# Optimization experiments

Measured on AMD Instinct MI355X. Metric: run time of the kernel, lower is better.

The kernel has to match this reference:

```python
import jax, jax.numpy as jnp
import numpy as np

EPS = 1e-12  # torch F.normalize clamp_min eps


def _agnn_conv(x, src, dst, beta, n):
    # x: [N, D]; src/dst: [E] (message flows src -> dst, softmax over dst's in-edges)
    xn = x / jnp.maximum(jnp.linalg.norm(x, axis=-1, keepdims=True), EPS)
    alpha = beta[0] * jnp.sum(xn[src] * xn[dst], axis=-1)            # [E] cosine sim * beta
    amax = jax.ops.segment_max(alpha, dst, num_segments=n)           # stable segment softmax
    ex = jnp.exp(alpha - amax[dst])
    denom = jax.ops.segment_sum(ex, dst, num_segments=n)
    w = ex / denom[dst]                                              # [E]
    return jax.ops.segment_sum(x[src] * w[:, None], dst, num_segments=n)


def setup_inputs() -> dict:
    key = jax.random.key(0)
    ks = jax.random.split(key, 8)
    N, E, G = 131072, 4194304, 2048
    x = jax.random.normal(ks[0], (N, 75), dtype=jnp.float32)
    edge_index = jax.random.randint(ks[1], (2, E), 0, N, dtype=jnp.int64)
    batch = jnp.sort(jax.random.randint(ks[2], (N,), 0, G, dtype=jnp.int64))
    lin1_w = jax.random.normal(ks[3], (16, 75), dtype=jnp.float32) * (1.0 / np.sqrt(75))
    lin1_b = jnp.zeros((16,), jnp.float32)
    beta1 = jnp.ones((1,), jnp.float32)   # prop1: requires_grad=False, beta=1
    beta2 = jnp.ones((1,), jnp.float32)   # prop2: learnable beta, init 1
    lin2_w = jax.random.normal(ks[4], (64, 16), dtype=jnp.float32) * (1.0 / np.sqrt(16))
    lin2_b = jnp.zeros((64,), jnp.float32)
    gather_w = jax.random.normal(ks[5], (1, 64), dtype=jnp.float32) * (1.0 / np.sqrt(64))
    gather_b = jnp.zeros((1,), jnp.float32)
    return {"x": x, "edge_index": edge_index, "batch": batch, "num_graphs": G,
            "lin1_w": lin1_w, "lin1_b": lin1_b, "beta1": beta1, "beta2": beta2,
            "lin2_w": lin2_w, "lin2_b": lin2_b, "gather_w": gather_w, "gather_b": gather_b}


def reference(x, edge_index, batch, num_graphs, lin1_w, lin1_b, beta1, beta2,
              lin2_w, lin2_b, gather_w, gather_b):
    n = x.shape[0]
    # PyG AGNNConv adds self-loops by default
    loops = jnp.arange(n, dtype=edge_index.dtype)
    src = jnp.concatenate([edge_index[0], loops])
    dst = jnp.concatenate([edge_index[1], loops])
    # dropout is identity in eval mode
    h = jax.nn.relu(x @ lin1_w.T + lin1_b)          # [N, 16]
    h = _agnn_conv(h, src, dst, beta1, n)
    h = _agnn_conv(h, src, dst, beta2, n)
    h = h @ lin2_w.T + lin2_b                        # [N, 64]
    y = jax.ops.segment_sum(h, batch, num_segments=num_graphs)  # global_add_pool [G, 64]
    return y @ gather_w.T + gather_b                 # [G, 1]
```

## Files before the change

kernel.cpp:

```cpp
#include <hip/hip_runtime.h>
#include <hip/hip_bf16.h>
#include <hip/hip_fp16.h>
#include <math.h>

#define SSEPS 1e-24f
#define NPB 256
#define NPB_SHIFT 8
#define SRC_BITS 17
#define SRC_MASK ((1 << SRC_BITS) - 1)
#define NB 512
#define CAP_B 8832
#define SC_EDGES 8192
#define SCB 512
#define SC_T 512
#define CSR_T 512

union QRowU { int2 v; _Float16 h[4]; };



__global__ void init_gcursor(int* g) {
    int i = threadIdx.x;
    if (i < NB) g[i] = i * CAP_B;
}

__global__ void init_out(float* out, const float* gb, int G) {
    int g = blockIdx.x * blockDim.x + threadIdx.x;
    if (g < G) out[g] = gb[0];
}

__global__ void compute_v(const float* l2w, const float* l2b, const float* gw,
                          float* vbuf) {
    int t = threadIdx.x;
    if (t < 16) {
        float a = 0.f;
        for (int j = 0; j < 64; ++j) a = fmaf(gw[j], l2w[j * 16 + t], a);
        vbuf[t] = a;
    } else if (t == 16) {
        float a = 0.f;
        for (int j = 0; j < 64; ++j) a = fmaf(gw[j], l2b[j], a);
        vbuf[16] = a;
    }
}

__global__ void lin1_relu(const float* __restrict__ x,
                          const float* __restrict__ W1,
                          const float* __restrict__ b1,
                          int* __restrict__ rec1, int N, int D) {
    __shared__ float Ws[16 * 75];
    __shared__ float Bs[16];
    for (int i = threadIdx.x; i < 16 * D; i += blockDim.x) Ws[i] = W1[i];
    if (threadIdx.x < 16) Bs[threadIdx.x] = b1[threadIdx.x];
    __syncthreads();

    int node = blockIdx.x * (blockDim.x >> 4) + (threadIdx.x >> 4);
    int c = threadIdx.x & 15;
    if (node >= N) return;

    const float* xr = x + (size_t)node * D;
    float acc = Bs[c];
    for (int k = 0; k < D; ++k) acc = fmaf(xr[k], Ws[c * D + k], acc);
    float h = fmaxf(acc, 0.f);

    float hn = __shfl_xor(h, 1);
    if (!(c & 1)) {
        union { _Float16 hh[2]; int i; } u;
        u.hh[0] = (_Float16)h;
        u.hh[1] = (_Float16)hn;
        rec1[8 * node + (c >> 1)] = u.i;
    }
}


__global__ __launch_bounds__(SC_T) void bucket_scatter(
    const int* __restrict__ src, const int* __restrict__ dst,
    int E, int* __restrict__ gcursor, int* __restrict__ packed) {
    __shared__ int lout[SC_EDGES];
    __shared__ int h[SCB];
    __shared__ int s[SCB];
    __shared__ int delta[SCB];
    int t = threadIdx.x;
    int base = blockIdx.x * SC_EDGES;
    int cnt = E - base;
    if (cnt > SC_EDGES) cnt = SC_EDGES;

    if (t < SCB) h[t] = 0;
    __syncthreads();
    for (int i = t; i < cnt; i += SC_T)
        atomicAdd(&h[dst[base + i] >> NPB_SHIFT], 1);
    __syncthreads();
    if (t < SCB) s[t] = h[t];
    __syncthreads();
    for (int off = 1; off < SCB; off <<= 1) {
        int a = (t < SCB && t >= off) ? s[t - off] : 0;
        __syncthreads();
        if (t < SCB) s[t] += a;
        __syncthreads();
    }
    if (t < SCB) {
        int c = h[t];
        int ex = s[t] - c;
        int gp = c ? atomicAdd(&gcursor[t], c) : 0;
        delta[t] = gp - ex;
        h[t] = ex;
    }
    __syncthreads();
    for (int i = t; i < cnt; i += SC_T) {
        int d = dst[base + i];
        int b = d >> NPB_SHIFT;
        int pos = atomicAdd(&h[b], 1);
        lout[pos] = ((d & (NPB - 1)) << SRC_BITS) | src[base + i];
    }
    __syncthreads();
    for (int i = t; i < cnt; i += SC_T) {
        int lo = 0, hi = SCB - 1;
        while (lo < hi) {
            int mid = (lo + hi) >> 1;
            if (s[mid] > i) hi = mid;
            else lo = mid + 1;
        }
        packed[delta[lo] + i] = lout[i];
    }
}

__global__ __launch_bounds__(CSR_T) void csr_build(
    const int* __restrict__ packed, const int* __restrict__ gcursor,
    int* __restrict__ deg, int* __restrict__ offs,
    int* __restrict__ csr_src, int N) {
    __shared__ int lout[CAP_B];
    __shared__ int ldeg[NPB];
    __shared__ int lofs[NPB];
    int b = blockIdx.x;
    int t = threadIdx.x;
    int e0 = b * CAP_B;
    int cnt = gcursor[b] - e0;
    if (t < NPB) ldeg[t] = 0;
    __syncthreads();
    for (int i = t; i < cnt; i += CSR_T)
        atomicAdd(&ldeg[packed[e0 + i] >> SRC_BITS], 1);
    __syncthreads();
    int v = (t < NPB) ? ldeg[t] : 0;
    if (t < NPB) lofs[t] = v;
    __syncthreads();
    for (int off = 1; off < NPB; off <<= 1) {
        int u = (t < NPB && t >= off) ? lofs[t - off] : 0;
        __syncthreads();
        if (t < NPB) lofs[t] += u;
        __syncthreads();
    }
    if (t < NPB) {
        int ex = lofs[t] - v;
        int node = (b << NPB_SHIFT) + t;
        if (node < N) {
            deg[node] = v;
            offs[node] = e0 + ex;
        }
        lofs[t] = ex;
    }
    __syncthreads();
    for (int i = t; i < cnt; i += CSR_T) {
        int p = packed[e0 + i];
        int pos = atomicAdd(&lofs[p >> SRC_BITS], 1);
        lout[pos] = p & SRC_MASK;
    }
    __syncthreads();
    for (int i = t; i < cnt; i += CSR_T)
        csr_src[e0 + i] = lout[i];
}

__global__ __launch_bounds__(256) void agnn_conv1(
    const int* __restrict__ rec1,
    const int* __restrict__ offs, const int* __restrict__ deg,
    const int* __restrict__ csr, const float* __restrict__ beta_p,
    int* __restrict__ rec2, int N) {
    int tid = blockIdx.x * blockDim.x + threadIdx.x;
    int node = tid >> 2;
    int q = tid & 3;
    if (node >= N) return;
    float beta = beta_p[0];
    const int2* rp = (const int2*)rec1;

    QRowU rdu;
    rdu.v = rp[4 * node + q];
    float xd[4];
#pragma unroll
    for (int k = 0; k < 4; ++k) xd[k] = (float)rdu.h[k];

    float ssd = 0.f;
#pragma unroll
    for (int k = 0; k < 4; ++k) ssd = fmaf(xd[k], xd[k], ssd);
    ssd += __shfl_xor(ssd, 1);
    ssd += __shfl_xor(ssd, 2);
    float invsd = rsqrtf(fmaxf(ssd, SSEPS));

    float e0 = __expf(beta * ssd * invsd * invsd);
    float denom = e0;
    float acc[4];
#pragma unroll
    for (int k = 0; k < 4; ++k) acc[k] = e0 * xd[k];

    int start = offs[node], cnt = deg[node];
    int i = 0;
    for (; i + 4 <= cnt; i += 4) {
        int j[4];
        QRowU r[4];
#pragma unroll
        for (int u = 0; u < 4; ++u) j[u] = __builtin_nontemporal_load(&csr[start + i + u]);
#pragma unroll
        for (int u = 0; u < 4; ++u) r[u].v = rp[4 * j[u] + q];
#pragma unroll
        for (int u = 0; u < 4; ++u) {
            float d = 0.f, ss = 0.f;
            float hs[4];
#pragma unroll
            for (int k = 0; k < 4; ++k) {
                hs[k] = (float)r[u].h[k];
                d = fmaf(xd[k], hs[k], d);
                ss = fmaf(hs[k], hs[k], ss);
            }
            d += __shfl_xor(d, 1);
            d += __shfl_xor(d, 2);
            ss += __shfl_xor(ss, 1);
            ss += __shfl_xor(ss, 2);
            float ee = __expf(beta * d * invsd * rsqrtf(fmaxf(ss, SSEPS)));
            denom += ee;
#pragma unroll
            for (int k = 0; k < 4; ++k) acc[k] = fmaf(ee, hs[k], acc[k]);
        }
    }
    for (; i < cnt; ++i) {
        int j = __builtin_nontemporal_load(&csr[start + i]);
        QRowU r;
        r.v = rp[4 * j + q];
        float d = 0.f, ss = 0.f;
        float hs[4];
#pragma unroll
        for (int k = 0; k < 4; ++k) {
            hs[k] = (float)r.h[k];
            d = fmaf(xd[k], hs[k], d);
            ss = fmaf(hs[k], hs[k], ss);
        }
        d += __shfl_xor(d, 1);
        d += __shfl_xor(d, 2);
        ss += __shfl_xor(ss, 1);
        ss += __shfl_xor(ss, 2);
        float ee = __expf(beta * d * invsd * rsqrtf(fmaxf(ss, SSEPS)));
        denom += ee;
#pragma unroll
        for (int k = 0; k < 4; ++k) acc[k] = fmaf(ee, hs[k], acc[k]);
    }

    float inv = 1.f / denom;
    QRowU w;
#pragma unroll
    for (int k = 0; k < 4; ++k) w.h[k] = (_Float16)(acc[k] * inv);
    ((int2*)rec2)[4 * node + q] = w.v;
}

__global__ __launch_bounds__(256) void agnn_conv2(
    const int* __restrict__ rec2,
    const int* __restrict__ offs, const int* __restrict__ deg,
    const int* __restrict__ csr, const float* __restrict__ beta_p,
    const float* __restrict__ vbuf,
    float* __restrict__ rbuf, int N) {
    int tid = blockIdx.x * blockDim.x + threadIdx.x;
    int node = tid >> 2;
    int q = tid & 3;
    if (node >= N) return;
    float beta = beta_p[0];
    const int2* rp = (const int2*)rec2;

    float vq[4];
#pragma unroll
    for (int k = 0; k < 4; ++k) vq[k] = vbuf[4 * q + k];

    QRowU rdu;
    rdu.v = rp[4 * node + q];
    float xd[4];
#pragma unroll
    for (int k = 0; k < 4; ++k) xd[k] = (float)rdu.h[k];

    float ssd = 0.f, pd = 0.f;
#pragma unroll
    for (int k = 0; k < 4; ++k) {
        ssd = fmaf(xd[k], xd[k], ssd);
        pd = fmaf(vq[k], xd[k], pd);
    }
    ssd += __shfl_xor(ssd, 1);
    ssd += __shfl_xor(ssd, 2);
    pd += __shfl_xor(pd, 1);
    pd += __shfl_xor(pd, 2);
    float invsd = rsqrtf(fmaxf(ssd, SSEPS));

    float e0 = __expf(beta * ssd * invsd * invsd);
    float denom = e0;
    float acc = e0 * pd;

    int start = offs[node], cnt = deg[node];
    int i = 0;
    for (; i + 4 <= cnt; i += 4) {
        int j[4];
        QRowU r[4];
#pragma unroll
        for (int u = 0; u < 4; ++u) j[u] = __builtin_nontemporal_load(&csr[start + i + u]);
#pragma unroll
        for (int u = 0; u < 4; ++u) r[u].v = rp[4 * j[u] + q];
#pragma unroll
        for (int u = 0; u < 4; ++u) {
            float d = 0.f, ss = 0.f, pv = 0.f;
#pragma unroll
            for (int k = 0; k < 4; ++k) {
                float hs = (float)r[u].h[k];
                d = fmaf(xd[k], hs, d);
                ss = fmaf(hs, hs, ss);
                pv = fmaf(vq[k], hs, pv);
            }
            d += __shfl_xor(d, 1);
            d += __shfl_xor(d, 2);
            ss += __shfl_xor(ss, 1);
            ss += __shfl_xor(ss, 2);
            pv += __shfl_xor(pv, 1);
            pv += __shfl_xor(pv, 2);
            float ee = __expf(beta * d * invsd * rsqrtf(fmaxf(ss, SSEPS)));
            denom += ee;
            acc = fmaf(ee, pv, acc);
        }
    }
    for (; i < cnt; ++i) {
        int j = __builtin_nontemporal_load(&csr[start + i]);
        QRowU r;
        r.v = rp[4 * j + q];
        float d = 0.f, ss = 0.f, pv = 0.f;
#pragma unroll
        for (int k = 0; k < 4; ++k) {
            float hs = (float)r.h[k];
            d = fmaf(xd[k], hs, d);
            ss = fmaf(hs, hs, ss);
            pv = fmaf(vq[k], hs, pv);
        }
        d += __shfl_xor(d, 1);
        d += __shfl_xor(d, 2);
        ss += __shfl_xor(ss, 1);
        ss += __shfl_xor(ss, 2);
        pv += __shfl_xor(pv, 1);
        pv += __shfl_xor(pv, 2);
        float ee = __expf(beta * d * invsd * rsqrtf(fmaxf(ss, SSEPS)));
        denom += ee;
        acc = fmaf(ee, pv, acc);
    }
    if (q == 0) rbuf[node] = acc / denom;
}

__global__ void pool_kernel(const float* __restrict__ r, const int* __restrict__ batch,
                            const float* __restrict__ vbuf, float* __restrict__ out,
                            int N) {
    int base = (blockIdx.x * blockDim.x + threadIdx.x) * 8;
    if (base >= N) return;
    float c0 = vbuf[16];
    int lim = base + 8;
    if (lim > N) lim = N;
    float run = 0.f;
    int g = -1;
    for (int i = base; i < lim; ++i) {
        int gi = batch[i];
        if (gi != g) {
            if (g >= 0) atomicAdd(&out[g], run);
            g = gi;
            run = 0.f;
        }
        run += r[i] + c0;
    }
    if (g >= 0) atomicAdd(&out[g], run);
}


extern "C" void kernel_launch(void* const* d_in, const int* in_sizes, int n_in,
                              void* d_out, int out_size, void* d_ws, size_t ws_size,
                              hipStream_t stream) {
    const float* x = (const float*)d_in[0];
    const int* edge_index = (const int*)d_in[1];
    const int* batch = (const int*)d_in[2];
    const float* lin1_w = (const float*)d_in[4];
    const float* lin1_b = (const float*)d_in[5];
    const float* beta1 = (const float*)d_in[6];
    const float* beta2 = (const float*)d_in[7];
    const float* lin2_w = (const float*)d_in[8];
    const float* lin2_b = (const float*)d_in[9];
    const float* gather_w = (const float*)d_in[10];
    const float* gather_b = (const float*)d_in[11];
    float* out = (float*)d_out;

    const int N = in_sizes[2];
    const int E = in_sizes[1] / 2;
    const int D = in_sizes[0] / N;
    const int G = out_size;

    const int* src = edge_index;
    const int* dst = edge_index + E;

    float* w = (float*)d_ws;
    int* rec1 = (int*)w;                 w += (size_t)N * 8;
    int* rec2 = (int*)w;                 w += (size_t)N * 8;
    float* rbuf = w;                     w += N;
    float* vbuf = w;                     w += 32;
    int* deg = (int*)w;                  w += N;
    int* offs = (int*)w;                 w += N;
    int* packed = (int*)w;               w += (size_t)NB * CAP_B;
    int* csr_src = (int*)w;              w += (size_t)NB * CAP_B;
    int* gcursor = (int*)w;              w += NB;

    const int B = 256;
    dim3 gridNode16((N + (B / 16) - 1) / (B / 16));
    dim3 gridNode4((4 * N + B - 1) / B);

    init_gcursor<<<dim3(1), NB, 0, stream>>>(gcursor);
    bucket_scatter<<<dim3((E + SC_EDGES - 1) / SC_EDGES), SC_T, 0, stream>>>(
        src, dst, E, gcursor, packed);
    csr_build<<<dim3(NB), CSR_T, 0, stream>>>(packed, gcursor, deg, offs, csr_src, N);

    lin1_relu<<<gridNode16, B, 0, stream>>>(x, lin1_w, lin1_b, rec1, N, D);
    compute_v<<<dim3(1), 64, 0, stream>>>(lin2_w, lin2_b, gather_w, vbuf);

    agnn_conv1<<<gridNode4, B, 0, stream>>>(rec1, offs, deg, csr_src,
                                            beta1, rec2, N);
    agnn_conv2<<<gridNode4, B, 0, stream>>>(rec2, offs, deg, csr_src,
                                            beta2, vbuf, rbuf, N);

    init_out<<<dim3((G + B - 1) / B), B, 0, stream>>>(out, gather_b, G);
    pool_kernel<<<dim3((N / 8 + B - 1) / B), B, 0, stream>>>(rbuf, batch, vbuf, out, N);
}
```

Before: 305.4 us.

## Sort nodes by in-degree and use two lanes per node with wider loads

Builds a degree histogram in csr_build, then scans it and scatters nodes into a degree-sorted permutation, so each wavefront in the AGNN conv kernels processes nodes of similar degree. This is meant to cut divergence and load imbalance inside a wavefront. The conv kernels also switch from 4 lanes x 8 bytes to 2 lanes x 16 bytes per node, with an unroll of 8 instead of 4, to issue fewer, wider gathers and fewer shuffles. In exchange it adds two small kernels and an indirection through perm, and the unroll of 8 raises register pressure.

Result: slower. 318.7 us (+4.4%).

```diff
diff --git a/kernel.cpp b/kernel.cpp
--- a/kernel.cpp
+++ b/kernel.cpp
@@ -14,14 +14,16 @@
 #define SCB 512
 #define SC_T 512
 #define CSR_T 512
-
-union QRowU { int2 v; _Float16 h[4]; };
-
-
-
-__global__ void init_gcursor(int* g) {
+#define DBINS 256
+
+union QRowU2 { int4 v; _Float16 h[8]; };
+
+
+
+__global__ void init_gcursor(int* g, int* hist) {
     int i = threadIdx.x;
     if (i < NB) g[i] = i * CAP_B;
+    if (i < DBINS) hist[i] = 0;
 }
 
 __global__ void init_out(float* out, const float* gb, int G) {
@@ -126,21 +128,24 @@
 __global__ __launch_bounds__(CSR_T) void csr_build(
     const int* __restrict__ packed, const int* __restrict__ gcursor,
     int* __restrict__ deg, int* __restrict__ offs,
-    int* __restrict__ csr_src, int N) {
+    int* __restrict__ csr_src, int* __restrict__ hist, int N) {
     __shared__ int lout[CAP_B];
     __shared__ int ldeg[NPB];
     __shared__ int lofs[NPB];
+    __shared__ int lhist[DBINS];
     int b = blockIdx.x;
     int t = threadIdx.x;
     int e0 = b * CAP_B;
     int cnt = gcursor[b] - e0;
     if (t < NPB) ldeg[t] = 0;
+    if (t < DBINS) lhist[t] = 0;
     __syncthreads();
     for (int i = t; i < cnt; i += CSR_T)
         atomicAdd(&ldeg[packed[e0 + i] >> SRC_BITS], 1);
     __syncthreads();
     int v = (t < NPB) ? ldeg[t] : 0;
     if (t < NPB) lofs[t] = v;
+    if (t < NPB) atomicAdd(&lhist[v < DBINS ? v : DBINS - 1], 1);
     __syncthreads();
     for (int off = 1; off < NPB; off <<= 1) {
         int u = (t < NPB && t >= off) ? lofs[t - off] : 0;
@@ -166,161 +171,197 @@
     __syncthreads();
     for (int i = t; i < cnt; i += CSR_T)
         csr_src[e0 + i] = lout[i];
+    if (t < DBINS && lhist[t]) atomicAdd(&hist[t], lhist[t]);
+}
+
+__global__ void deg_scan(const int* __restrict__ hist, int* __restrict__ cursor) {
+    __shared__ int s[DBINS];
+    int t = threadIdx.x;
+    int h = hist[t];
+    s[t] = h;
+    __syncthreads();
+    for (int off = 1; off < DBINS; off <<= 1) {
+        int a = (t >= off) ? s[t - off] : 0;
+        __syncthreads();
+        s[t] += a;
+        __syncthreads();
+    }
+    cursor[t] = s[t] - h;
+}
+
+__global__ void deg_scatter(const int* __restrict__ deg, const int* __restrict__ offs,
+                            int* __restrict__ cursor, int* __restrict__ perm,
+                            int* __restrict__ sdeg, int* __restrict__ soffs, int N) {
+    __shared__ int lh[DBINS];
+    __shared__ int lb[DBINS];
+    int t = threadIdx.x;
+    if (t < DBINS) lh[t] = 0;
+    __syncthreads();
+    int i = blockIdx.x * blockDim.x + t;
+    int bin = 0, r = 0, dv = 0;
+    if (i < N) {
+        dv = deg[i];
+        bin = dv < DBINS ? dv : DBINS - 1;
+        r = atomicAdd(&lh[bin], 1);
+    }
+    __syncthreads();
+    if (t < DBINS && lh[t]) lb[t] = atomicAdd(&cursor[t], lh[t]);
+    __syncthreads();
+    if (i < N) {
+        int p = lb[bin] + r;
+        perm[p] = i;
+        sdeg[p] = dv;
+        soffs[p] = offs[i];
+    }
 }
 
 __global__ __launch_bounds__(256) void agnn_conv1(
     const int* __restrict__ rec1,
-    const int* __restrict__ offs, const int* __restrict__ deg,
-    const int* __restrict__ csr, const float* __restrict__ beta_p,
+    const int* __restrict__ soffs, const int* __restrict__ sdeg,
+    const int* __restrict__ csr, const int* __restrict__ perm,
+    const float* __restrict__ beta_p,
     int* __restrict__ rec2, int N) {
     int tid = blockIdx.x * blockDim.x + threadIdx.x;
-    int node = tid >> 2;
-    int q = tid & 3;
-    if (node >= N) return;
+    int slot = tid >> 1;
+    int q = tid & 1;
+    if (slot >= N) return;
+    int node = perm[slot];
     float beta = beta_p[0];
-    const int2* rp = (const int2*)rec1;
-
-    QRowU rdu;
-    rdu.v = rp[4 * node + q];
-    float xd[4];
-#pragma unroll
-    for (int k = 0; k < 4; ++k) xd[k] = (float)rdu.h[k];
+    const int4* rp = (const int4*)rec1;
+
+    QRowU2 rdu;
+    rdu.v = rp[2 * node + q];
+    float xd[8];
+#pragma unroll
+    for (int k = 0; k < 8; ++k) xd[k] = (float)rdu.h[k];
 
     float ssd = 0.f;
 #pragma unroll
-    for (int k = 0; k < 4; ++k) ssd = fmaf(xd[k], xd[k], ssd);
+    for (int k = 0; k < 8; ++k) ssd = fmaf(xd[k], xd[k], ssd);
     ssd += __shfl_xor(ssd, 1);
-    ssd += __shfl_xor(ssd, 2);
     float invsd = rsqrtf(fmaxf(ssd, SSEPS));
 
     float e0 = __expf(beta * ssd * invsd * invsd);
     float denom = e0;
-    float acc[4];
-#pragma unroll
-    for (int k = 0; k < 4; ++k) acc[k] = e0 * xd[k];
-
-    int start = offs[node], cnt = deg[node];
+    float acc[8];
+#pragma unroll
+    for (int k = 0; k < 8; ++k) acc[k] = e0 * xd[k];
+
+    int start = soffs[slot], cnt = sdeg[slot];
     int i = 0;
-    for (; i + 4 <= cnt; i += 4) {
-        int j[4];
-        QRowU r[4];
-#pragma unroll
-        for (int u = 0; u < 4; ++u) j[u] = __builtin_nontemporal_load(&csr[start + i + u]);
-#pragma unroll
-        for (int u = 0; u < 4; ++u) r[u].v = rp[4 * j[u] + q];
-#pragma unroll
-        for (int u = 0; u < 4; ++u) {
+    for (; i + 8 <= cnt; i += 8) {
+        int j[8];
+        QRowU2 r[8];
+#pragma unroll
+        for (int u = 0; u < 8; ++u) j[u] = __builtin_nontemporal_load(&csr[start + i + u]);
+#pragma unroll
+        for (int u = 0; u < 8; ++u) r[u].v = rp[2 * j[u] + q];
+#pragma unroll
+        for (int u = 0; u < 8; ++u) {
             float d = 0.f, ss = 0.f;
-            float hs[4];
-#pragma unroll
-            for (int k = 0; k < 4; ++k) {
+            float hs[8];
+#pragma unroll
+            for (int k = 0; k < 8; ++k) {
                 hs[k] = (float)r[u].h[k];
                 d = fmaf(xd[k], hs[k], d);
                 ss = fmaf(hs[k], hs[k], ss);
             }
             d += __shfl_xor(d, 1);
-            d += __shfl_xor(d, 2);
             ss += __shfl_xor(ss, 1);
-            ss += __shfl_xor(ss, 2);
             float ee = __expf(beta * d * invsd * rsqrtf(fmaxf(ss, SSEPS)));
             denom += ee;
 #pragma unroll
-            for (int k = 0; k < 4; ++k) acc[k] = fmaf(ee, hs[k], acc[k]);
+            for (int k = 0; k < 8; ++k) acc[k] = fmaf(ee, hs[k], acc[k]);
         }
     }
     for (; i < cnt; ++i) {
         int j = __builtin_nontemporal_load(&csr[start + i]);
-        QRowU r;
-        r.v = rp[4 * j + q];
+        QRowU2 r;
+        r.v = rp[2 * j + q];
         float d = 0.f, ss = 0.f;
-        float hs[4];
-#pragma unroll
-        for (int k = 0; k < 4; ++k) {
+        float hs[8];
+#pragma unroll
+        for (int k = 0; k < 8; ++k) {
             hs[k] = (float)r.h[k];
             d = fmaf(xd[k], hs[k], d);
             ss = fmaf(hs[k], hs[k], ss);
         }
         d += __shfl_xor(d, 1);
-        d += __shfl_xor(d, 2);
         ss += __shfl_xor(ss, 1);
-        ss += __shfl_xor(ss, 2);
         float ee = __expf(beta * d * invsd * rsqrtf(fmaxf(ss, SSEPS)));
         denom += ee;
 #pragma unroll
-        for (int k = 0; k < 4; ++k) acc[k] = fmaf(ee, hs[k], acc[k]);
+        for (int k = 0; k < 8; ++k) acc[k] = fmaf(ee, hs[k], acc[k]);
     }
 
     float inv = 1.f / denom;
-    QRowU w;
-#pragma unroll
-    for (int k = 0; k < 4; ++k) w.h[k] = (_Float16)(acc[k] * inv);
-    ((int2*)rec2)[4 * node + q] = w.v;
+    QRowU2 w;
+#pragma unroll
+    for (int k = 0; k < 8; ++k) w.h[k] = (_Float16)(acc[k] * inv);
+    ((int4*)rec2)[2 * node + q] = w.v;
 }
 
 __global__ __launch_bounds__(256) void agnn_conv2(
     const int* __restrict__ rec2,
-    const int* __restrict__ offs, const int* __restrict__ deg,
-    const int* __restrict__ csr, const float* __restrict__ beta_p,
+    const int* __restrict__ soffs, const int* __restrict__ sdeg,
+    const int* __restrict__ csr, const int* __restrict__ perm,
+    const float* __restrict__ beta_p,
     const float* __restrict__ vbuf,
     float* __restrict__ rbuf, int N) {
     int tid = blockIdx.x * blockDim.x + threadIdx.x;
-    int node = tid >> 2;
-    int q = tid & 3;
-    if (node >= N) return;
+    int slot = tid >> 1;
+    int q = tid & 1;
+    if (slot >= N) return;
+    int node = perm[slot];
     float beta = beta_p[0];
-    const int2* rp = (const int2*)rec2;
-
-    float vq[4];
-#pragma unroll
-    for (int k = 0; k < 4; ++k) vq[k] = vbuf[4 * q + k];
-
-    QRowU rdu;
-    rdu.v = rp[4 * node + q];
-    float xd[4];
-#pragma unroll
-    for (int k = 0; k < 4; ++k) xd[k] = (float)rdu.h[k];
+    const int4* rp = (const int4*)rec2;
+
+    float vq[8];
+#pragma unroll
+    for (int k = 0; k < 8; ++k) vq[k] = vbuf[8 * q + k];
+
+    QRowU2 rdu;
+    rdu.v = rp[2 * node + q];
+    float xd[8];
+#pragma unroll
+    for (int k = 0; k < 8; ++k) xd[k] = (float)rdu.h[k];
 
     float ssd = 0.f, pd = 0.f;
 #pragma unroll
-    for (int k = 0; k < 4; ++k) {
+    for (int k = 0; k < 8; ++k) {
         ssd = fmaf(xd[k], xd[k], ssd);
         pd = fmaf(vq[k], xd[k], pd);
     }
     ssd += __shfl_xor(ssd, 1);
-    ssd += __shfl_xor(ssd, 2);
     pd += __shfl_xor(pd, 1);
-    pd += __shfl_xor(pd, 2);
     float invsd = rsqrtf(fmaxf(ssd, SSEPS));
 
     float e0 = __expf(beta * ssd * invsd * invsd);
     float denom = e0;
     float acc = e0 * pd;
 
-    int start = offs[node], cnt = deg[node];
+    int start = soffs[slot], cnt = sdeg[slot];
     int i = 0;
-    for (; i + 4 <= cnt; i += 4) {
-        int j[4];
-        QRowU r[4];
-#pragma unroll
-        for (int u = 0; u < 4; ++u) j[u] = __builtin_nontemporal_load(&csr[start + i + u]);
-#pragma unroll
-        for (int u = 0; u < 4; ++u) r[u].v = rp[4 * j[u] + q];
-#pragma unroll
-        for (int u = 0; u < 4; ++u) {
+    for (; i + 8 <= cnt; i += 8) {
+        int j[8];
+        QRowU2 r[8];
+#pragma unroll
+        for (int u = 0; u < 8; ++u) j[u] = __builtin_nontemporal_load(&csr[start + i + u]);
+#pragma unroll
+        for (int u = 0; u < 8; ++u) r[u].v = rp[2 * j[u] + q];
+#pragma unroll
+        for (int u = 0; u < 8; ++u) {
             float d = 0.f, ss = 0.f, pv = 0.f;
 #pragma unroll
-            for (int k = 0; k < 4; ++k) {
+            for (int k = 0; k < 8; ++k) {
                 float hs = (float)r[u].h[k];
                 d = fmaf(xd[k], hs, d);
                 ss = fmaf(hs, hs, ss);
                 pv = fmaf(vq[k], hs, pv);
             }
             d += __shfl_xor(d, 1);
-            d += __shfl_xor(d, 2);
             ss += __shfl_xor(ss, 1);
-            ss += __shfl_xor(ss, 2);
             pv += __shfl_xor(pv, 1);
-            pv += __shfl_xor(pv, 2);
             float ee = __expf(beta * d * invsd * rsqrtf(fmaxf(ss, SSEPS)));
             denom += ee;
             acc = fmaf(ee, pv, acc);
@@ -328,22 +369,19 @@
     }
     for (; i < cnt; ++i) {
         int j = __builtin_nontemporal_load(&csr[start + i]);
-        QRowU r;
-        r.v = rp[4 * j + q];
+        QRowU2 r;
+        r.v = rp[2 * j + q];
         float d = 0.f, ss = 0.f, pv = 0.f;
 #pragma unroll
-        for (int k = 0; k < 4; ++k) {
+        for (int k = 0; k < 8; ++k) {
             float hs = (float)r.h[k];
             d = fmaf(xd[k], hs, d);
             ss = fmaf(hs, hs, ss);
             pv = fmaf(vq[k], hs, pv);
         }
         d += __shfl_xor(d, 1);
-        d += __shfl_xor(d, 2);
         ss += __shfl_xor(ss, 1);
-        ss += __shfl_xor(ss, 2);
         pv += __shfl_xor(pv, 1);
-        pv += __shfl_xor(pv, 2);
         float ee = __expf(beta * d * invsd * rsqrtf(fmaxf(ss, SSEPS)));
         denom += ee;
         acc = fmaf(ee, pv, acc);
@@ -408,22 +446,32 @@
     int* packed = (int*)w;               w += (size_t)NB * CAP_B;
     int* csr_src = (int*)w;              w += (size_t)NB * CAP_B;
     int* gcursor = (int*)w;              w += NB;
+    int* perm = (int*)w;                 w += N;
+    int* sdeg = (int*)w;                 w += N;
+    int* soffs = (int*)w;                w += N;
+    int* hist = (int*)w;                 w += DBINS;
+    int* cursor = (int*)w;               w += DBINS;
 
     const int B = 256;
     dim3 gridNode16((N + (B / 16) - 1) / (B / 16));
-    dim3 gridNode4((4 * N + B - 1) / B);
-
-    init_gcursor<<<dim3(1), NB, 0, stream>>>(gcursor);
+    dim3 gridNode2((2 * N + B - 1) / B);
+
+    init_gcursor<<<dim3(1), NB, 0, stream>>>(gcursor, hist);
     bucket_scatter<<<dim3((E + SC_EDGES - 1) / SC_EDGES), SC_T, 0, stream>>>(
         src, dst, E, gcursor, packed);
-    csr_build<<<dim3(NB), CSR_T, 0, stream>>>(packed, gcursor, deg, offs, csr_src, N);
+    csr_build<<<dim3(NB), CSR_T, 0, stream>>>(packed, gcursor, deg, offs, csr_src,
+                                              hist, N);
+
+    deg_scan<<<dim3(1), DBINS, 0, stream>>>(hist, cursor);
+    deg_scatter<<<dim3((N + B - 1) / B), B, 0, stream>>>(deg, offs, cursor, perm,
+                                                         sdeg, soffs, N);
 
     lin1_relu<<<gridNode16, B, 0, stream>>>(x, lin1_w, lin1_b, rec1, N, D);
     compute_v<<<dim3(1), 64, 0, stream>>>(lin2_w, lin2_b, gather_w, vbuf);
 
-    agnn_conv1<<<gridNode4, B, 0, stream>>>(rec1, offs, deg, csr_src,
+    agnn_conv1<<<gridNode2, B, 0, stream>>>(rec1, soffs, sdeg, csr_src, perm,
                                             beta1, rec2, N);
-    agnn_conv2<<<gridNode4, B, 0, stream>>>(rec2, offs, deg, csr_src,
+    agnn_conv2<<<gridNode2, B, 0, stream>>>(rec2, soffs, sdeg, csr_src, perm,
                                             beta2, vbuf, rbuf, N);
 
     init_out<<<dim3((G + B - 1) / B), B, 0, stream>>>(out, gather_b, G);
```
